# Kernel optimization log

Hardware: AMD Instinct MI355X
Metric: run time of the kernel (lower is better)

## Reference

```python
import jax, jax.numpy as jnp
import numpy as np

B = 128          # batch
T = 196          # total_patches per view (2 views -> 2*T tokens)
ENC = 1024       # encoder_embed_dim
DEC = 512        # decoder_embed_dim
V = 98           # num unmasked (visible) tokens per sample
M = 2 * T - V    # num masked tokens (294)


def setup_inputs() -> dict:
    key = jax.random.key(0)
    kx, kperm, kw, kmt, kpos, kview = jax.random.split(key, 6)
    x = jax.random.normal(kx, (B, V, ENC), jnp.float32)
    # masked_ids: unique ids per row in [0, 2T) — built from permutations
    perms = jax.vmap(jax.random.permutation, in_axes=(0, None))(
        jax.random.split(kperm, B), 2 * T)
    masked_ids = perms[:, :M].astype(jnp.int64)
    W = jax.random.normal(kw, (DEC, ENC), jnp.float32) * 0.02
    b = jnp.zeros((DEC,), jnp.float32)
    mask_token = jax.random.normal(kmt, (1, 1, DEC), jnp.float32)
    pos_embed = jax.random.normal(kpos, (1, 2 * T, DEC), jnp.float32)
    view_embed = jax.random.normal(kview, (2, DEC), jnp.float32)
    return {"x": x, "masked_ids": masked_ids, "W": W, "b": b,
            "mask_token": mask_token, "pos_embed": pos_embed,
            "view_embed": view_embed}


def reference(x, masked_ids, W, b, mask_token, pos_embed, view_embed):
    Bn = x.shape[0]
    # Linear: enc -> dec
    xp = jnp.einsum('bve,de->bvd', x, W) + b          # (B, V, DEC)
    # visible ids = sorted complement of masked_ids (vectorized, no batch loop)
    rows = jnp.arange(Bn)[:, None]
    vis_mask = jnp.ones((Bn, 2 * T), bool).at[rows, masked_ids].set(False)
    # stable argsort puts True(visible, ~mask=False) positions first, in order
    visible_ids = jnp.argsort(~vis_mask, axis=1)[:, :V]  # (B, V)
    # scatter projected visible tokens into mask-token placeholders
    base = jnp.broadcast_to(mask_token, (Bn, 2 * T, DEC))
    view = base.at[rows, visible_ids].set(xp)          # (B, 2T, DEC)
    # per-view embedding: first T tokens -> view 0, last T -> view 1
    ve = jnp.concatenate([
        jnp.broadcast_to(view_embed[0], (T, DEC)),
        jnp.broadcast_to(view_embed[1], (T, DEC))], axis=0)  # (2T, DEC)
    return view + pos_embed + ve[None, :, :]
```

## Files before the change

### kernel.cpp

```cpp
#include <hip/hip_runtime.h>

#define BATCH 128
#define VIS   98
#define TOK   196
#define TOK2  392
#define ENC   1024
#define DEC   512
#define MSK   294

#define NXB 6272
#define NWB 256
#define NFILL 1176

#define NGEMM 784

typedef __bf16 bf16x8 __attribute__((ext_vector_type(8)));
typedef float  f32x4  __attribute__((ext_vector_type(4)));

__device__ __forceinline__ unsigned short f2bf(float f) {
    union { float f; unsigned u; } c; c.f = f;
    unsigned u = c.u;
    return (unsigned short)((u + 0x7fffu + ((u >> 16) & 1u)) >> 16);
}

__device__ __forceinline__ void g2lds16(const void* gptr, void* lptr) {
    __builtin_amdgcn_global_load_lds(
        (const __attribute__((address_space(1))) void*)gptr,
        (__attribute__((address_space(3))) void*)lptr, 16, 0, 0);
}

__global__ __launch_bounds__(512) void setup_fill(
    const float* __restrict__ x,
    const float* __restrict__ W,
    const int* __restrict__ mids,
    const float* __restrict__ mask_token,
    const float* __restrict__ pos,
    const float* __restrict__ ve,
    unsigned short* __restrict__ xb,
    unsigned short* __restrict__ wbm,
    int* __restrict__ visids,
    float* __restrict__ out) {
    int bid = blockIdx.x, tid = threadIdx.x;
    if (bid < NXB + NWB) {
        const float* src = (bid < NXB) ? x : W;
        unsigned short* dst = (bid < NXB) ? xb : wbm;
        int i = (bid < NXB ? bid : bid - NXB) * 512 + tid;
        float4 f = ((const float4*)src)[i];
        ushort4 o;
        o.x = f2bf(f.x); o.y = f2bf(f.y); o.z = f2bf(f.z); o.w = f2bf(f.w);
        ((ushort4*)dst)[i] = o;
        return;
    }
    if (bid < NXB + NWB + BATCH) {
        int b = bid - NXB - NWB;
        __shared__ unsigned char lf[TOK2];
        __shared__ int wtot[8];
        if (tid < TOK2) lf[tid] = 1;
        __syncthreads();
        if (tid < MSK) lf[mids[b * MSK + tid]] = 0;
        __syncthreads();
        int flag = (tid < TOK2) ? (int)lf[tid] : 0;
        unsigned long long bal = __ballot(flag != 0);
        int lane = tid & 63, wv = tid >> 6;
        int pre = __popcll(bal & ((1ull << lane) - 1ull));
        if (lane == 0) wtot[wv] = __popcll(bal);
        __syncthreads();
        int off = 0;
        for (int i = 0; i < wv; ++i) off += wtot[i];
        if (flag) visids[b * VIS + off + pre] = tid;
        return;
    }
    int fb = bid - (NXB + NWB + BATCH);
    __shared__ int base[32];
    __shared__ int tsl[32];
    if (tid < 32) {
        int fid = fb * 32 + tid;
        int b = fid / MSK;
        int t = mids[fid];
        tsl[tid] = t;
        base[tid] = (b * TOK2 + t) * 128;
    }
    __syncthreads();
    float4 m = ((const float4*)mask_token)[tid & 127];
    #pragma unroll
    for (int i = 0; i < 8; ++i) {
        int g = i * 512 + tid;
        int ltok = g >> 7;
        int d4 = tid & 127;
        int t = tsl[ltok];
        float4 p = ((const float4*)pos)[t * 128 + d4];
        float4 v = ((const float4*)(ve + (t >= TOK ? DEC : 0)))[d4];
        float4 r;
        r.x = m.x + p.x + v.x;
        r.y = m.y + p.y + v.y;
        r.z = m.z + p.z + v.z;
        r.w = m.w + p.w + v.w;
        ((float4*)out)[base[ltok] + d4] = r;
    }
}

__global__ __launch_bounds__(256, 4) void gemm_scatter(
    const unsigned short* __restrict__ xb,
    const unsigned short* __restrict__ wb,
    const float* __restrict__ bias,
    const float* __restrict__ pos,
    const float* __restrict__ ve,
    const int* __restrict__ vis,
    float* __restrict__ out) {
    __shared__ unsigned short As[64 * 64];
    __shared__ unsigned short Bs[128 * 64];
    __shared__ int rowdst[64];
    __shared__ int rowt[64];

    int bid = blockIdx.x;
    int tid = threadIdx.x;
    int lane = tid & 63, w = tid >> 6;
    int l16 = lane & 15, q = lane >> 4;
    int wm = w & 1, wn = w >> 1;

    int mb, nb;
    if (bid < 768) { mb = (bid & 7) + ((bid >> 5) << 3); nb = (bid >> 3) & 3; }
    else           { int ii = bid - 768; mb = 192 + (ii & 3); nb = ii >> 2; }
    int m0 = mb * 64, n0 = nb * 128;

    if (tid < 64) {
        int gr = m0 + tid;
        int t = vis[gr];
        rowt[tid] = t;
        rowdst[tid] = (gr / VIS) * TOK2 + t;
    }

    int c = (tid & 7) ^ ((tid >> 3) & 7);
    const unsigned short* gA = xb + (size_t)(m0 + (tid >> 3)) * ENC + c * 8;
    const unsigned short* gB = wb + (size_t)(n0 + (tid >> 3)) * ENC + c * 8;
    char* ldsA = (char*)As + tid * 16;
    char* ldsB = (char*)Bs + tid * 16;

    f32x4 acc[2][4];
    #pragma unroll
    for (int i = 0; i < 2; ++i)
        #pragma unroll
        for (int j = 0; j < 4; ++j)
            acc[i][j] = (f32x4){0.f, 0.f, 0.f, 0.f};

    for (int k0 = 0; k0 < ENC; k0 += 64) {
        __syncthreads();
        #pragma unroll
        for (int t = 0; t < 2; ++t)
            g2lds16(gA + (size_t)t * 32 * ENC + k0, ldsA + t * 4096);
        #pragma unroll
        for (int t = 0; t < 4; ++t)
            g2lds16(gB + (size_t)t * 32 * ENC + k0, ldsB + t * 4096);
        __syncthreads();

        #pragma unroll
        for (int u = 0; u < 2; ++u) {
            int slot = ((u * 4 + q) ^ (l16 & 7)) * 16;
            bf16x8 bfrag[4], afrag[2];
            #pragma unroll
            for (int j = 0; j < 4; ++j)
                bfrag[j] = *(const bf16x8*)((const char*)Bs + (wn * 64 + j * 16 + l16) * 128 + slot);
            #pragma unroll
            for (int i = 0; i < 2; ++i)
                afrag[i] = *(const bf16x8*)((const char*)As + (wm * 32 + i * 16 + l16) * 128 + slot);
            #pragma unroll
            for (int i = 0; i < 2; ++i)
                #pragma unroll
                for (int j = 0; j < 4; ++j)
                    acc[i][j] = __builtin_amdgcn_mfma_f32_16x16x32_bf16(afrag[i], bfrag[j], acc[i][j], 0, 0, 0);
        }
    }

    #pragma unroll
    for (int j = 0; j < 4; ++j) {
        int gcol = n0 + wn * 64 + j * 16 + l16;
        float bc = bias[gcol];
        float v0 = ve[gcol];
        float v1 = ve[DEC + gcol];
        #pragma unroll
        for (int i = 0; i < 2; ++i) {
            #pragma unroll
            for (int r = 0; r < 4; ++r) {
                int rl = wm * 32 + i * 16 + q * 4 + r;
                int t = rowt[rl];
                float val = acc[i][j][r] + bc + pos[(size_t)t * DEC + gcol]
                          + (t >= TOK ? v1 : v0);
                out[(size_t)rowdst[rl] * DEC + gcol] = val;
            }
        }
    }
}

extern "C" void kernel_launch(void* const* d_in, const int* in_sizes, int n_in,
                              void* d_out, int out_size, void* d_ws, size_t ws_size,
                              hipStream_t stream) {
    (void)in_sizes; (void)n_in; (void)out_size; (void)ws_size;
    const float* x    = (const float*)d_in[0];
    const int*   mids = (const int*)d_in[1];
    const float* W    = (const float*)d_in[2];
    const float* bias = (const float*)d_in[3];
    const float* mt   = (const float*)d_in[4];
    const float* pos  = (const float*)d_in[5];
    const float* ve   = (const float*)d_in[6];
    float* out = (float*)d_out;

    unsigned short* xb = (unsigned short*)d_ws;
    unsigned short* wbm = xb + (size_t)BATCH * VIS * ENC;
    int* visids = (int*)(wbm + (size_t)DEC * ENC);

    hipLaunchKernelGGL(setup_fill, dim3(NXB + NWB + BATCH + NFILL), dim3(512), 0, stream,
                       x, W, mids, mt, pos, ve, xb, wbm, visids, out);
    hipLaunchKernelGGL(gemm_scatter, dim3(NGEMM), dim3(256), 0, stream,
                       xb, wbm, bias, pos, ve, visids, out);
}
```

Baseline: 178.9 us.

## Fuse x fp32-to-bf16 conversion into GEMM with full-N tiles and double-buffered W

The separate pass that converts x to bf16 in workspace is removed. The GEMM now reads fp32 x directly, converts it into LDS in two halves of K, and computes a full 64x512 output tile per 512-thread block. W tiles are double-buffered with async global-to-LDS loads and explicit waitcnt and barriers. This avoids writing and re-reading a 25 MB bf16 copy of x, but it drops the grid to 196 blocks with large LDS use, which may underfill the GPU's compute units.

```diff
diff --git a/kernel.cpp b/kernel.cpp
--- a/kernel.cpp
+++ b/kernel.cpp
@@ -8,11 +8,9 @@
 #define DEC   512
 #define MSK   294
 
-#define NXB 6272
 #define NWB 256
 #define NFILL 1176
-
-#define NGEMM 784
+#define NGEMM 196
 
 typedef __bf16 bf16x8 __attribute__((ext_vector_type(8)));
 typedef float  f32x4  __attribute__((ext_vector_type(4)));
@@ -30,29 +28,25 @@
 }
 
 __global__ __launch_bounds__(512) void setup_fill(
-    const float* __restrict__ x,
     const float* __restrict__ W,
     const int* __restrict__ mids,
     const float* __restrict__ mask_token,
     const float* __restrict__ pos,
     const float* __restrict__ ve,
-    unsigned short* __restrict__ xb,
     unsigned short* __restrict__ wbm,
     int* __restrict__ visids,
     float* __restrict__ out) {
     int bid = blockIdx.x, tid = threadIdx.x;
-    if (bid < NXB + NWB) {
-        const float* src = (bid < NXB) ? x : W;
-        unsigned short* dst = (bid < NXB) ? xb : wbm;
-        int i = (bid < NXB ? bid : bid - NXB) * 512 + tid;
-        float4 f = ((const float4*)src)[i];
+    if (bid < NWB) {
+        int i = bid * 512 + tid;
+        float4 f = ((const float4*)W)[i];
         ushort4 o;
         o.x = f2bf(f.x); o.y = f2bf(f.y); o.z = f2bf(f.z); o.w = f2bf(f.w);
-        ((ushort4*)dst)[i] = o;
+        ((ushort4*)wbm)[i] = o;
         return;
     }
-    if (bid < NXB + NWB + BATCH) {
-        int b = bid - NXB - NWB;
+    if (bid < NWB + BATCH) {
+        int b = bid - NWB;
         __shared__ unsigned char lf[TOK2];
         __shared__ int wtot[8];
         if (tid < TOK2) lf[tid] = 1;
@@ -70,7 +64,7 @@
         if (flag) visids[b * VIS + off + pre] = tid;
         return;
     }
-    int fb = bid - (NXB + NWB + BATCH);
+    int fb = bid - (NWB + BATCH);
     __shared__ int base[32];
     __shared__ int tsl[32];
     if (tid < 32) {
@@ -99,29 +93,48 @@
     }
 }
 
-__global__ __launch_bounds__(256, 4) void gemm_scatter(
-    const unsigned short* __restrict__ xb,
+__device__ __forceinline__ void convertA(const float* __restrict__ gx,
+                                         unsigned short* __restrict__ As,
+                                         int tid, int h) {
+    int cr = tid >> 3, cj = tid & 7;
+    const float* src = gx + (size_t)cr * ENC + h * 512;
+    float4 f[16];
+    #pragma unroll
+    for (int kk = 0; kk < 8; ++kk) {
+        const float4* p = (const float4*)(src + (cj + 8 * kk) * 8);
+        f[2 * kk]     = p[0];
+        f[2 * kk + 1] = p[1];
+    }
+    #pragma unroll
+    for (int kk = 0; kk < 8; ++kk) {
+        int c = cj + 8 * kk;
+        bf16x8 v;
+        v[0] = (__bf16)f[2*kk].x;   v[1] = (__bf16)f[2*kk].y;
+        v[2] = (__bf16)f[2*kk].z;   v[3] = (__bf16)f[2*kk].w;
+        v[4] = (__bf16)f[2*kk+1].x; v[5] = (__bf16)f[2*kk+1].y;
+        v[6] = (__bf16)f[2*kk+1].z; v[7] = (__bf16)f[2*kk+1].w;
+        *(bf16x8*)((char*)As + cr * 1024 + ((c ^ (cr & 7)) * 16)) = v;
+    }
+}
+
+__global__ __launch_bounds__(512, 2) void gemm_conv(
+    const float* __restrict__ x,
     const unsigned short* __restrict__ wb,
     const float* __restrict__ bias,
     const float* __restrict__ pos,
     const float* __restrict__ ve,
     const int* __restrict__ vis,
     float* __restrict__ out) {
-    __shared__ unsigned short As[64 * 64];
-    __shared__ unsigned short Bs[128 * 64];
+    __shared__ unsigned short As[64 * 512];
+    __shared__ unsigned short Bs[2][512 * 32];
     __shared__ int rowdst[64];
     __shared__ int rowt[64];
 
-    int bid = blockIdx.x;
-    int tid = threadIdx.x;
+    int bid = blockIdx.x, tid = threadIdx.x;
     int lane = tid & 63, w = tid >> 6;
     int l16 = lane & 15, q = lane >> 4;
     int wm = w & 1, wn = w >> 1;
-
-    int mb, nb;
-    if (bid < 768) { mb = (bid & 7) + ((bid >> 5) << 3); nb = (bid >> 3) & 3; }
-    else           { int ii = bid - 768; mb = 192 + (ii & 3); nb = ii >> 2; }
-    int m0 = mb * 64, n0 = nb * 128;
+    int m0 = bid * 64;
 
     if (tid < 64) {
         int gr = m0 + tid;
@@ -130,50 +143,72 @@
         rowdst[tid] = (gr / VIS) * TOK2 + t;
     }
 
-    int c = (tid & 7) ^ ((tid >> 3) & 7);
-    const unsigned short* gA = xb + (size_t)(m0 + (tid >> 3)) * ENC + c * 8;
-    const unsigned short* gB = wb + (size_t)(n0 + (tid >> 3)) * ENC + c * 8;
-    char* ldsA = (char*)As + tid * 16;
-    char* ldsB = (char*)Bs + tid * 16;
-
-    f32x4 acc[2][4];
+    const unsigned short* gBbase = wb + (size_t)(tid >> 2) * ENC
+                                      + (((tid & 3) ^ ((tid >> 3) & 3)) * 8);
+    const float* gx = x + (size_t)m0 * ENC;
+
+    f32x4 acc[2][8];
     #pragma unroll
     for (int i = 0; i < 2; ++i)
         #pragma unroll
-        for (int j = 0; j < 4; ++j)
+        for (int j = 0; j < 8; ++j)
             acc[i][j] = (f32x4){0.f, 0.f, 0.f, 0.f};
 
-    for (int k0 = 0; k0 < ENC; k0 += 64) {
-        __syncthreads();
-        #pragma unroll
-        for (int t = 0; t < 2; ++t)
-            g2lds16(gA + (size_t)t * 32 * ENC + k0, ldsA + t * 4096);
-        #pragma unroll
-        for (int t = 0; t < 4; ++t)
-            g2lds16(gB + (size_t)t * 32 * ENC + k0, ldsB + t * 4096);
-        __syncthreads();
-
-        #pragma unroll
-        for (int u = 0; u < 2; ++u) {
-            int slot = ((u * 4 + q) ^ (l16 & 7)) * 16;
-            bf16x8 bfrag[4], afrag[2];
+    #pragma unroll
+    for (int qq = 0; qq < 4; ++qq)
+        g2lds16(gBbase + (size_t)qq * 128 * ENC,
+                (char*)(&Bs[0][0]) + qq * 8192 + tid * 16);
+    convertA(gx, As, tid, 0);
+    __syncthreads();
+
+    for (int s = 0; s < 32; ++s) {
+        int buf = s & 1;
+        if (s < 31) {
+            int k0 = (s + 1) * 32;
             #pragma unroll
-            for (int j = 0; j < 4; ++j)
-                bfrag[j] = *(const bf16x8*)((const char*)Bs + (wn * 64 + j * 16 + l16) * 128 + slot);
+            for (int qq = 0; qq < 4; ++qq)
+                g2lds16(gBbase + (size_t)qq * 128 * ENC + k0,
+                        (char*)(&Bs[buf ^ 1][0]) + qq * 8192 + tid * 16);
+            __builtin_amdgcn_sched_barrier(0);
+            asm volatile("s_waitcnt vmcnt(4)" ::: "memory");
+        } else {
+            __builtin_amdgcn_sched_barrier(0);
+            asm volatile("s_waitcnt vmcnt(0)" ::: "memory");
+        }
+        __builtin_amdgcn_s_barrier();
+        __builtin_amdgcn_sched_barrier(0);
+
+        int sl = s & 15;
+        const char* Bb = (const char*)(&Bs[buf][0]);
+        bf16x8 afrag[2], bfrag[8];
+        #pragma unroll
+        for (int i = 0; i < 2; ++i) {
+            int row = wm * 32 + i * 16 + l16;
+            afrag[i] = *(const bf16x8*)((const char*)As + row * 1024
+                        + (((sl * 4 + q) ^ (l16 & 7)) * 16));
+        }
+        #pragma unroll
+        for (int j = 0; j < 8; ++j) {
+            int col = wn * 128 + j * 16 + l16;
+            bfrag[j] = *(const bf16x8*)(Bb + col * 64
+                        + ((q ^ ((col >> 1) & 3)) * 16));
+        }
+        #pragma unroll
+        for (int i = 0; i < 2; ++i)
             #pragma unroll
-            for (int i = 0; i < 2; ++i)
-                afrag[i] = *(const bf16x8*)((const char*)As + (wm * 32 + i * 16 + l16) * 128 + slot);
-            #pragma unroll
-            for (int i = 0; i < 2; ++i)
-                #pragma unroll
-                for (int j = 0; j < 4; ++j)
-                    acc[i][j] = __builtin_amdgcn_mfma_f32_16x16x32_bf16(afrag[i], bfrag[j], acc[i][j], 0, 0, 0);
-        }
-    }
-
-    #pragma unroll
-    for (int j = 0; j < 4; ++j) {
-        int gcol = n0 + wn * 64 + j * 16 + l16;
+            for (int j = 0; j < 8; ++j)
+                acc[i][j] = __builtin_amdgcn_mfma_f32_16x16x32_bf16(afrag[i], bfrag[j], acc[i][j], 0, 0, 0);
+        __builtin_amdgcn_s_barrier();
+
+        if (s == 15) {
+            convertA(gx, As, tid, 1);
+            __syncthreads();
+        }
+    }
+
+    #pragma unroll
+    for (int j = 0; j < 8; ++j) {
+        int gcol = wn * 128 + j * 16 + l16;
         float bc = bias[gcol];
         float v0 = ve[gcol];
         float v1 = ve[DEC + gcol];
@@ -204,12 +239,11 @@
     const float* ve   = (const float*)d_in[6];
     float* out = (float*)d_out;
 
-    unsigned short* xb = (unsigned short*)d_ws;
-    unsigned short* wbm = xb + (size_t)BATCH * VIS * ENC;
+    unsigned short* wbm = (unsigned short*)d_ws;
     int* visids = (int*)(wbm + (size_t)DEC * ENC);
 
-    hipLaunchKernelGGL(setup_fill, dim3(NXB + NWB + BATCH + NFILL), dim3(512), 0, stream,
-                       x, W, mids, mt, pos, ve, xb, wbm, visids, out);
-    hipLaunchKernelGGL(gemm_scatter, dim3(NGEMM), dim3(256), 0, stream,
-                       xb, wbm, bias, pos, ve, visids, out);
-}
+    hipLaunchKernelGGL(setup_fill, dim3(NWB + BATCH + NFILL), dim3(512), 0, stream,
+                       W, mids, mt, pos, ve, wbm, visids, out);
+    hipLaunchKernelGGL(gemm_conv, dim3(NGEMM), dim3(512), 0, stream,
+                       x, wbm, bias, pos, ve, visids, out);
+}
```

Result: slower. 187.5 us (+4.8%).
